# Kernel tuning notes

Measured on AMD Instinct MI355X. Metric: run time of the kernel, lower is better.

Reference implementation:

```python
import jax, jax.numpy as jnp
import numpy as np

MARGIN = 1.0
EPS = 1e-08


def setup_inputs() -> dict:
    key = jax.random.key(0)
    k0, k1 = jax.random.split(key)
    kernels0 = jax.random.normal(k0, (2048, 3, 3), dtype=jnp.float32)
    kernels1 = jax.random.normal(k1, (1024, 5, 5), dtype=jnp.float32)
    return {"kernels0": kernels0, "kernels1": kernels1}


def _layer_loss(kernels):
    n, d, _ = kernels.shape
    # Frobenius-normalize each kernel
    norms = jnp.sqrt(jnp.sum(kernels * kernels, axis=(1, 2), keepdims=True)) + EPS
    kn = kernels / norms                      # (n, d, d)
    inv = jnp.linalg.inv(kn)                  # (n, d, d)
    # AB[i, j] = inv[i] @ kn[j]; BA[i, j] = inv[j] @ kn[i]
    ab = jnp.einsum('iab,jbc->ijac', inv, kn)  # (n, n, d, d)
    ba = jnp.einsum('jab,ibc->ijac', inv, kn)  # (n, n, d, d)
    eye = jnp.eye(d, dtype=kernels.dtype)
    diff_ab = jnp.sqrt(jnp.sum((eye - ab) ** 2, axis=(2, 3)))  # (n, n)
    diff_ba = jnp.sqrt(jnp.sum((eye - ba) ** 2, axis=(2, 3)))  # (n, n)
    combined = jnp.tril(diff_ab) + jnp.triu(diff_ba)
    loss_mat = jax.nn.relu(MARGIN - combined)
    mask = ~jnp.eye(n, dtype=bool)
    loss_mat = jnp.where(mask, loss_mat, 0.0)
    return jnp.sum(loss_mat) / (n * (n - 1))


def reference(kernels0, kernels1):
    losses = [_layer_loss(kernels0), _layer_loss(kernels1)]
    return sum(losses) / len(losses)
```

## Files before the change

kernel.cpp:

```cpp
#include <hip/hip_runtime.h>
#include <math.h>

#define N0 2048
#define N1 1024
#define M0T 32
#define M1T 32
#define NB0 (M0T * (M0T + 1) / 2)
#define NB1 (M1T * (M1T + 1) / 2)
#define NBLK0 (2 * NB0)
#define NBLK1 (2 * NB1)
#define NBTOT (NBLK0 + NBLK1)


__device__ __forceinline__ void tri_decode(int t, int& bi, int& bj) {
    int b = (int)((sqrtf(8.0f * t + 1.0f) - 1.0f) * 0.5f);
    while ((b + 1) * (b + 2) / 2 <= t) ++b;
    while (b * (b + 1) / 2 > t) --b;
    bi = b;
    bj = t - b * (b + 1) / 2;
}

__device__ __forceinline__ void inv3_to(const float* __restrict__ g, float* __restrict__ dst) {
    float a[9];
    float ss = 0.0f;
#pragma unroll
    for (int e = 0; e < 9; ++e) { a[e] = g[e]; ss = fmaf(a[e], a[e], ss); }
    float rn = 1.0f / (sqrtf(ss) + 1e-8f);
#pragma unroll
    for (int e = 0; e < 9; ++e) a[e] *= rn;
    float c00 = a[4] * a[8] - a[5] * a[7];
    float c01 = -(a[3] * a[8] - a[5] * a[6]);
    float c02 = a[3] * a[7] - a[4] * a[6];
    float det = a[0] * c00 + a[1] * c01 + a[2] * c02;
    float id = 1.0f / det;
    float x[9];
    x[0] = c00 * id;
    x[1] = (a[2] * a[7] - a[1] * a[8]) * id;
    x[2] = (a[1] * a[5] - a[2] * a[4]) * id;
    x[3] = c01 * id;
    x[4] = (a[0] * a[8] - a[2] * a[6]) * id;
    x[5] = (a[2] * a[3] - a[0] * a[5]) * id;
    x[6] = c02 * id;
    x[7] = (a[1] * a[6] - a[0] * a[7]) * id;
    x[8] = (a[0] * a[4] - a[1] * a[3]) * id;
    float r[9];
#pragma unroll
    for (int i = 0; i < 3; ++i)
#pragma unroll
        for (int j = 0; j < 3; ++j) {
            float m = a[i * 3 + 0] * x[0 * 3 + j];
            m = fmaf(a[i * 3 + 1], x[1 * 3 + j], m);
            m = fmaf(a[i * 3 + 2], x[2 * 3 + j], m);
            r[i * 3 + j] = ((i == j) ? 2.0f : 0.0f) - m;
        }
#pragma unroll
    for (int i = 0; i < 3; ++i)
#pragma unroll
        for (int j = 0; j < 3; ++j) {
            float m = x[i * 3 + 0] * r[0 * 3 + j];
            m = fmaf(x[i * 3 + 1], r[1 * 3 + j], m);
            m = fmaf(x[i * 3 + 2], r[2 * 3 + j], m);
            dst[i * 3 + j] = m;
        }
}

__device__ __forceinline__ void norm3_to(const float* __restrict__ g, float* __restrict__ dst) {
    float a[9];
    float ss = 0.0f;
#pragma unroll
    for (int e = 0; e < 9; ++e) { a[e] = g[e]; ss = fmaf(a[e], a[e], ss); }
    float rn = 1.0f / (sqrtf(ss) + 1e-8f);
#pragma unroll
    for (int e = 0; e < 9; ++e) dst[e] = a[e] * rn;
}

__device__ __forceinline__ void inv5_to(const float* __restrict__ g, float* __restrict__ dst) {
    float A[5][5], B[5][5], K[5][5];
    float ss = 0.0f;
#pragma unroll
    for (int r = 0; r < 5; ++r)
#pragma unroll
        for (int c = 0; c < 5; ++c) {
            float v = g[r * 5 + c];
            A[r][c] = v;
            ss = fmaf(v, v, ss);
        }
    float rn = 1.0f / (sqrtf(ss) + 1e-8f);
#pragma unroll
    for (int r = 0; r < 5; ++r)
#pragma unroll
        for (int c = 0; c < 5; ++c) {
            A[r][c] *= rn;
            K[r][c] = A[r][c];
            B[r][c] = (r == c) ? 1.0f : 0.0f;
        }
#pragma unroll
    for (int k = 0; k < 5; ++k) {
#pragma unroll
        for (int r = k + 1; r < 5; ++r) {
            bool sw = fabsf(A[r][k]) > fabsf(A[k][k]);
#pragma unroll
            for (int c = k; c < 5; ++c) {
                float Ar = A[r][c], Ak = A[k][c];
                A[r][c] = sw ? Ak : Ar;
                A[k][c] = sw ? Ar : Ak;
            }
#pragma unroll
            for (int c = 0; c < 5; ++c) {
                float Br = B[r][c], Bk = B[k][c];
                B[r][c] = sw ? Bk : Br;
                B[k][c] = sw ? Br : Bk;
            }
        }
        float piv = 1.0f / A[k][k];
#pragma unroll
        for (int c = k; c < 5; ++c) A[k][c] *= piv;
#pragma unroll
        for (int c = 0; c < 5; ++c) B[k][c] *= piv;
#pragma unroll
        for (int r = 0; r < 5; ++r) {
            if (r == k) continue;
            float f = A[r][k];
#pragma unroll
            for (int c = k; c < 5; ++c) A[r][c] = fmaf(-f, A[k][c], A[r][c]);
#pragma unroll
            for (int c = 0; c < 5; ++c) B[r][c] = fmaf(-f, B[k][c], B[r][c]);
        }
    }
    float R[5][5];
#pragma unroll
    for (int i = 0; i < 5; ++i)
#pragma unroll
        for (int j = 0; j < 5; ++j) {
            float m = K[i][0] * B[0][j];
#pragma unroll
            for (int k = 1; k < 5; ++k) m = fmaf(K[i][k], B[k][j], m);
            R[i][j] = ((i == j) ? 2.0f : 0.0f) - m;
        }
#pragma unroll
    for (int i = 0; i < 5; ++i)
#pragma unroll
        for (int j = 0; j < 5; ++j) {
            float m = B[i][0] * R[0][j];
#pragma unroll
            for (int k = 1; k < 5; ++k) m = fmaf(B[i][k], R[k][j], m);
            dst[i * 5 + j] = m;
        }
}

__device__ __forceinline__ void norm5_to(const float* __restrict__ g, float* __restrict__ dst) {
    float a[25];
    float ss = 0.0f;
#pragma unroll
    for (int e = 0; e < 25; ++e) { a[e] = g[e]; ss = fmaf(a[e], a[e], ss); }
    float rn = 1.0f / (sqrtf(ss) + 1e-8f);
#pragma unroll
    for (int e = 0; e < 25; ++e) dst[e] = a[e] * rn;
}

__global__ __launch_bounds__(256) void pairs_kernel(const float* __restrict__ k0,
                                                    const float* __restrict__ k1,
                                                    float* __restrict__ partial) {
    __shared__ __align__(16) float sA[800];
    __shared__ __align__(16) float sB[400];
    int tid = threadIdx.x;
    float contrib = 0.0f;

    if (blockIdx.x < NBLK0) {
        int t = blockIdx.x;
        int pb = t >> 1, h = t & 1;
        int bi, bj;
        tri_decode(pb, bi, bj);

        if (tid < 64) {
            inv3_to(k0 + (bi * 64 + tid) * 9, sA + tid * 9);
        } else if (tid < 96) {
            int j = tid - 64;
            norm3_to(k0 + (bj * 64 + h * 32 + j) * 9, sB + j * 9);
        }
        __syncthreads();

        int ti = tid >> 4, tj = tid & 15;
        int ibase = bi * 64 + ti * 4;
        int jbase = bj * 64 + h * 32 + tj * 2;
        float a[4][9];
#pragma unroll
        for (int u = 0; u < 4; ++u)
#pragma unroll
            for (int e = 0; e < 9; ++e) a[u][e] = sA[(ti * 4 + u) * 9 + e];
#pragma unroll
        for (int v = 0; v < 2; ++v) {
            float b[9];
#pragma unroll
            for (int e = 0; e < 9; ++e) b[e] = sB[(tj * 2 + v) * 9 + e];
#pragma unroll
            for (int u = 0; u < 4; ++u) {
                float s = 0.0f;
#pragma unroll
                for (int r = 0; r < 3; ++r)
#pragma unroll
                    for (int c = 0; c < 3; ++c) {
                        float m = a[u][r * 3 + 0] * b[c];
                        m = fmaf(a[u][r * 3 + 1], b[3 + c], m);
                        m = fmaf(a[u][r * 3 + 2], b[6 + c], m);
                        float d = ((r == c) ? 1.0f : 0.0f) - m;
                        s = fmaf(d, d, s);
                    }
                bool take = ((ibase + u) > (jbase + v)) && (s < 1.0f);
                contrib += take ? (1.0f - __builtin_amdgcn_sqrtf(s)) : 0.0f;
            }
        }
    } else {
        int t = blockIdx.x - NBLK0;
        int pb = t >> 1, h = t & 1;
        int bi, bj;
        tri_decode(pb, bi, bj);

        if (tid < 32) {
            inv5_to(k1 + (bi * 32 + tid) * 25, sA + tid * 25);
        } else if (tid < 48) {
            int j = tid - 32;
            norm5_to(k1 + (bj * 32 + h * 16 + j) * 25, sB + j * 25);
        }
        __syncthreads();

        int ti = tid >> 4, tj = tid & 15;
        int ibase = bi * 32 + ti * 2;
        int j = bj * 32 + h * 16 + tj;
        float a[2][25];
#pragma unroll
        for (int u = 0; u < 2; ++u)
#pragma unroll
            for (int e = 0; e < 25; ++e) a[u][e] = sA[(ti * 2 + u) * 25 + e];
        float b[25];
#pragma unroll
        for (int e = 0; e < 25; ++e) b[e] = sB[tj * 25 + e];
#pragma unroll
        for (int u = 0; u < 2; ++u) {
            float s = 0.0f;
#pragma unroll
            for (int r = 0; r < 5; ++r)
#pragma unroll
                for (int c = 0; c < 5; ++c) {
                    float m = a[u][r * 5 + 0] * b[c];
#pragma unroll
                    for (int k = 1; k < 5; ++k) m = fmaf(a[u][r * 5 + k], b[k * 5 + c], m);
                    float d = ((r == c) ? 1.0f : 0.0f) - m;
                    s = fmaf(d, d, s);
                }
            bool take = ((ibase + u) > j) && (s < 1.0f);
            contrib += take ? (1.0f - __builtin_amdgcn_sqrtf(s)) : 0.0f;
        }
    }

#pragma unroll
    for (int off = 32; off; off >>= 1) contrib += __shfl_down(contrib, off);
    __shared__ float wsum[4];
    if ((tid & 63) == 0) wsum[tid >> 6] = contrib;
    __syncthreads();
    if (tid == 0) partial[blockIdx.x] = wsum[0] + wsum[1] + wsum[2] + wsum[3];
}

__global__ void finalize_kernel(const float* __restrict__ partial, float* __restrict__ out) {
    int tid = threadIdx.x;
    double s0 = 0.0, s1 = 0.0;
    for (int x = tid; x < NBLK0; x += 256) s0 += (double)partial[x];
    for (int x = NBLK0 + tid; x < NBTOT; x += 256) s1 += (double)partial[x];
#pragma unroll
    for (int off = 32; off; off >>= 1) {
        s0 += __shfl_down(s0, off);
        s1 += __shfl_down(s1, off);
    }
    __shared__ double w0[4], w1[4];
    if ((tid & 63) == 0) { w0[tid >> 6] = s0; w1[tid >> 6] = s1; }
    __syncthreads();
    if (tid == 0) {
        double S0 = w0[0] + w0[1] + w0[2] + w0[3];
        double S1 = w1[0] + w1[1] + w1[2] + w1[3];
        double res = S0 / ((double)N0 * (double)(N0 - 1)) +
                     S1 / ((double)N1 * (double)(N1 - 1));
        out[0] = (float)res;
    }
}

extern "C" void kernel_launch(void* const* d_in, const int* in_sizes, int n_in,
                              void* d_out, int out_size, void* d_ws, size_t ws_size,
                              hipStream_t stream) {
    const float* k0 = (const float*)d_in[0];
    const float* k1 = (const float*)d_in[1];
    float* out = (float*)d_out;

    float* partial = (float*)d_ws;

    pairs_kernel<<<NBTOT, 256, 0, stream>>>(k0, k1, partial);
    finalize_kernel<<<1, 256, 0, stream>>>(partial, out);
}
```

Baseline: 69.91 us.

## Merge half-tile blocks into full tiles and drop 5x5 inverse refinement

Each block now covers a full 64x64 (3x3 layer) or 32x32 (5x5 layer) tile pair instead of splitting it into two half-blocks. This halves the block count and redundant inverse computations, and doubles per-thread register work. The Newton-Schulz refinement step after Gauss-Jordan elimination in the 5x5 inverse is removed, cutting serial work in the prologue but risking slightly less accurate inverses for ill-conditioned kernels. The grid shrinks to ~1056 blocks with more work per thread, which may lower occupancy and load balance.

New measurement: 65.36 us. -6.5%, faster.

```diff
diff --git a/kernel.cpp b/kernel.cpp
--- a/kernel.cpp
+++ b/kernel.cpp
@@ -7,9 +7,7 @@
 #define M1T 32
 #define NB0 (M0T * (M0T + 1) / 2)
 #define NB1 (M1T * (M1T + 1) / 2)
-#define NBLK0 (2 * NB0)
-#define NBLK1 (2 * NB1)
-#define NBTOT (NBLK0 + NBLK1)
+#define NBTOT (NB0 + NB1)
 
 
 __device__ __forceinline__ void tri_decode(int t, int& bi, int& bj) {
@@ -75,7 +73,7 @@
 }
 
 __device__ __forceinline__ void inv5_to(const float* __restrict__ g, float* __restrict__ dst) {
-    float A[5][5], B[5][5], K[5][5];
+    float A[5][5], B[5][5];
     float ss = 0.0f;
 #pragma unroll
     for (int r = 0; r < 5; ++r)
@@ -91,7 +89,6 @@
 #pragma unroll
         for (int c = 0; c < 5; ++c) {
             A[r][c] *= rn;
-            K[r][c] = A[r][c];
             B[r][c] = (r == c) ? 1.0f : 0.0f;
         }
 #pragma unroll
@@ -127,25 +124,10 @@
             for (int c = 0; c < 5; ++c) B[r][c] = fmaf(-f, B[k][c], B[r][c]);
         }
     }
-    float R[5][5];
-#pragma unroll
-    for (int i = 0; i < 5; ++i)
-#pragma unroll
-        for (int j = 0; j < 5; ++j) {
-            float m = K[i][0] * B[0][j];
-#pragma unroll
-            for (int k = 1; k < 5; ++k) m = fmaf(K[i][k], B[k][j], m);
-            R[i][j] = ((i == j) ? 2.0f : 0.0f) - m;
-        }
-#pragma unroll
-    for (int i = 0; i < 5; ++i)
-#pragma unroll
-        for (int j = 0; j < 5; ++j) {
-            float m = B[i][0] * R[0][j];
-#pragma unroll
-            for (int k = 1; k < 5; ++k) m = fmaf(B[i][k], R[k][j], m);
-            dst[i * 5 + j] = m;
-        }
+#pragma unroll
+    for (int r = 0; r < 5; ++r)
+#pragma unroll
+        for (int c = 0; c < 5; ++c) dst[r * 5 + c] = B[r][c];
 }
 
 __device__ __forceinline__ void norm5_to(const float* __restrict__ g, float* __restrict__ dst) {
@@ -162,37 +144,34 @@
                                                     const float* __restrict__ k1,
                                                     float* __restrict__ partial) {
     __shared__ __align__(16) float sA[800];
-    __shared__ __align__(16) float sB[400];
+    __shared__ __align__(16) float sB[800];
     int tid = threadIdx.x;
     float contrib = 0.0f;
 
-    if (blockIdx.x < NBLK0) {
-        int t = blockIdx.x;
-        int pb = t >> 1, h = t & 1;
+    if (blockIdx.x < NB0) {
         int bi, bj;
-        tri_decode(pb, bi, bj);
+        tri_decode(blockIdx.x, bi, bj);
 
         if (tid < 64) {
             inv3_to(k0 + (bi * 64 + tid) * 9, sA + tid * 9);
-        } else if (tid < 96) {
+        } else if (tid < 128) {
             int j = tid - 64;
-            norm3_to(k0 + (bj * 64 + h * 32 + j) * 9, sB + j * 9);
+            norm3_to(k0 + (bj * 64 + j) * 9, sB + j * 9);
         }
         __syncthreads();
 
         int ti = tid >> 4, tj = tid & 15;
-        int ibase = bi * 64 + ti * 4;
-        int jbase = bj * 64 + h * 32 + tj * 2;
+        int ibase = bi * 64 + ti * 4, jbase = bj * 64 + tj * 4;
         float a[4][9];
 #pragma unroll
         for (int u = 0; u < 4; ++u)
 #pragma unroll
             for (int e = 0; e < 9; ++e) a[u][e] = sA[(ti * 4 + u) * 9 + e];
 #pragma unroll
-        for (int v = 0; v < 2; ++v) {
+        for (int v = 0; v < 4; ++v) {
             float b[9];
 #pragma unroll
-            for (int e = 0; e < 9; ++e) b[e] = sB[(tj * 2 + v) * 9 + e];
+            for (int e = 0; e < 9; ++e) b[e] = sB[(tj * 4 + v) * 9 + e];
 #pragma unroll
             for (int u = 0; u < 4; ++u) {
                 float s = 0.0f;
@@ -211,45 +190,45 @@
             }
         }
     } else {
-        int t = blockIdx.x - NBLK0;
-        int pb = t >> 1, h = t & 1;
         int bi, bj;
-        tri_decode(pb, bi, bj);
+        tri_decode(blockIdx.x - NB0, bi, bj);
 
         if (tid < 32) {
             inv5_to(k1 + (bi * 32 + tid) * 25, sA + tid * 25);
-        } else if (tid < 48) {
+        } else if (tid < 64) {
             int j = tid - 32;
-            norm5_to(k1 + (bj * 32 + h * 16 + j) * 25, sB + j * 25);
+            norm5_to(k1 + (bj * 32 + j) * 25, sB + j * 25);
         }
         __syncthreads();
 
         int ti = tid >> 4, tj = tid & 15;
-        int ibase = bi * 32 + ti * 2;
-        int j = bj * 32 + h * 16 + tj;
+        int ibase = bi * 32 + ti * 2, jbase = bj * 32 + tj * 2;
         float a[2][25];
 #pragma unroll
         for (int u = 0; u < 2; ++u)
 #pragma unroll
             for (int e = 0; e < 25; ++e) a[u][e] = sA[(ti * 2 + u) * 25 + e];
-        float b[25];
-#pragma unroll
-        for (int e = 0; e < 25; ++e) b[e] = sB[tj * 25 + e];
-#pragma unroll
-        for (int u = 0; u < 2; ++u) {
-            float s = 0.0f;
-#pragma unroll
-            for (int r = 0; r < 5; ++r)
-#pragma unroll
-                for (int c = 0; c < 5; ++c) {
-                    float m = a[u][r * 5 + 0] * b[c];
-#pragma unroll
-                    for (int k = 1; k < 5; ++k) m = fmaf(a[u][r * 5 + k], b[k * 5 + c], m);
-                    float d = ((r == c) ? 1.0f : 0.0f) - m;
-                    s = fmaf(d, d, s);
-                }
-            bool take = ((ibase + u) > j) && (s < 1.0f);
-            contrib += take ? (1.0f - __builtin_amdgcn_sqrtf(s)) : 0.0f;
+#pragma unroll
+        for (int v = 0; v < 2; ++v) {
+            float b[25];
+#pragma unroll
+            for (int e = 0; e < 25; ++e) b[e] = sB[(tj * 2 + v) * 25 + e];
+#pragma unroll
+            for (int u = 0; u < 2; ++u) {
+                float s = 0.0f;
+#pragma unroll
+                for (int r = 0; r < 5; ++r)
+#pragma unroll
+                    for (int c = 0; c < 5; ++c) {
+                        float m = a[u][r * 5 + 0] * b[c];
+#pragma unroll
+                        for (int k = 1; k < 5; ++k) m = fmaf(a[u][r * 5 + k], b[k * 5 + c], m);
+                        float d = ((r == c) ? 1.0f : 0.0f) - m;
+                        s = fmaf(d, d, s);
+                    }
+                bool take = ((ibase + u) > (jbase + v)) && (s < 1.0f);
+                contrib += take ? (1.0f - __builtin_amdgcn_sqrtf(s)) : 0.0f;
+            }
         }
     }
 
@@ -264,8 +243,8 @@
 __global__ void finalize_kernel(const float* __restrict__ partial, float* __restrict__ out) {
     int tid = threadIdx.x;
     double s0 = 0.0, s1 = 0.0;
-    for (int x = tid; x < NBLK0; x += 256) s0 += (double)partial[x];
-    for (int x = NBLK0 + tid; x < NBTOT; x += 256) s1 += (double)partial[x];
+    for (int x = tid; x < NB0; x += 256) s0 += (double)partial[x];
+    for (int x = NB0 + tid; x < NBTOT; x += 256) s1 += (double)partial[x];
 #pragma unroll
     for (int off = 32; off; off >>= 1) {
         s0 += __shfl_down(s0, off);
```
